# Kernel tuning notes

Hardware: AMD Instinct MI355X
Metric: run time of the kernel (lower is better)

The kernel has to match this reference:

```python
import jax, jax.numpy as jnp
import numpy as np

N = 100000      # nodes
E = 1600000     # edges
R = 8           # relations
D_IN = 64
D_H = 64
D_OUT = 64
G = 64          # graphs in batch


def setup_inputs() -> dict:
    key = jax.random.key(0)
    ks = jax.random.split(key, 10)
    x = jax.random.normal(ks[0], (N, D_IN), dtype=jnp.float32)
    edge_index = jax.random.randint(ks[1], (2, E), 0, N, dtype=jnp.int32)
    edge_type = jax.random.randint(ks[2], (E,), 0, R, dtype=jnp.int32)
    batch = jnp.sort(jax.random.randint(ks[3], (N,), 0, G, dtype=jnp.int32))
    s1 = 1.0 / np.sqrt(D_IN)
    s2 = 1.0 / np.sqrt(D_H)
    W1 = jax.random.normal(ks[4], (R, D_IN, D_H), dtype=jnp.float32) * s1
    root1 = jax.random.normal(ks[5], (D_IN, D_H), dtype=jnp.float32) * s1
    b1 = jnp.zeros((D_H,), dtype=jnp.float32)
    W2 = jax.random.normal(ks[6], (R, D_H, D_OUT), dtype=jnp.float32) * s2
    root2 = jax.random.normal(ks[7], (D_H, D_OUT), dtype=jnp.float32) * s2
    b2 = jnp.zeros((D_OUT,), dtype=jnp.float32)
    return {"x": x, "edge_index": edge_index, "edge_type": edge_type, "batch": batch,
            "W1": W1, "root1": root1, "b1": b1, "W2": W2, "root2": root2, "b2": b2}


def _rgcn_conv(x, src, dst, etype, W, root, b):
    # PyG RGCNConv (num_bases=None, aggr='mean'):
    #   out_i = sum_r mean_{j in N_r(i)} x_j @ W_r + x_i @ root + b
    # Aggregate-then-transform: per-(dst, relation) mean of source features,
    # then one einsum over relation weights.
    num_nodes, d = x.shape
    num_rel = W.shape[0]
    seg = dst * num_rel + etype                          # composite (node, rel) id
    sums = jax.ops.segment_sum(x[src], seg, num_segments=num_nodes * num_rel)
    cnt = jax.ops.segment_sum(jnp.ones_like(seg, dtype=x.dtype), seg,
                              num_segments=num_nodes * num_rel)
    mean = sums / jnp.maximum(cnt, 1.0)[:, None]         # [N*R, d]
    mean = mean.reshape(num_nodes, num_rel, d)           # [N, R, d]
    return jnp.einsum('nrd,rdh->nh', mean, W) + x @ root + b


def reference(x, edge_index, edge_type, batch, W1, root1, b1, W2, root2, b2):
    src, dst = edge_index[0], edge_index[1]
    h = jax.nn.relu(_rgcn_conv(x, src, dst, edge_type, W1, root1, b1))
    h = _rgcn_conv(h, src, dst, edge_type, W2, root2, b2)
    # global_mean_pool over graph ids
    gsum = jax.ops.segment_sum(h, batch, num_segments=G)
    gcnt = jax.ops.segment_sum(jnp.ones((h.shape[0],), h.dtype), batch, num_segments=G)
    return gsum / jnp.maximum(gcnt, 1.0)[:, None]
```

## Files before the change

kernel.cpp:

```cpp
#include <hip/hip_runtime.h>
#include <stdint.h>

typedef __attribute__((ext_vector_type(8))) short short8;
typedef __attribute__((ext_vector_type(4))) float floatx4;

__device__ inline float bf2f(unsigned short u) {
  union { unsigned int i; float f; } v; v.i = ((unsigned int)u) << 16; return v.f;
}
__device__ inline unsigned short f2bf(float f) {
  union { float f; unsigned int i; } v; v.f = f;
  unsigned int r = v.i + 0x7FFFu + ((v.i >> 16) & 1u);
  return (unsigned short)(r >> 16);
}

__global__ void zero_i32(int* __restrict__ p, int n) {
  int i = blockIdx.x * blockDim.x + threadIdx.x;
  if (i < n) p[i] = 0;
}

__global__ void count_rank(const int* __restrict__ dst, const int* __restrict__ et,
                           int* __restrict__ cnt, unsigned short* __restrict__ rank,
                           int E) {
  int e = blockIdx.x * blockDim.x + threadIdx.x;
  if (e < E) {
    int idx = dst[e] * 8 + et[e];
    rank[e] = (unsigned short)atomicAdd(&cnt[idx], 1);
  }
}

__global__ void invert_cnt(const int* __restrict__ cnt, float* __restrict__ inv, int n) {
  int i = blockIdx.x * blockDim.x + threadIdx.x;
  if (i < n) inv[i] = 1.0f / fmaxf((float)cnt[i], 1.0f);
}

#define SCAN_T 256
#define SCAN_E 4

__global__ void scan1(const int* __restrict__ cnt, int* __restrict__ bsum, int n) {
  __shared__ int lds[SCAN_T];
  int base = blockIdx.x * (SCAN_T * SCAN_E);
  int tid = threadIdx.x;
  int s = 0;
#pragma unroll
  for (int j = 0; j < SCAN_E; ++j) {
    int i = base + tid * SCAN_E + j;
    if (i < n) s += cnt[i];
  }
  lds[tid] = s; __syncthreads();
  for (int off = SCAN_T / 2; off > 0; off >>= 1) {
    if (tid < off) lds[tid] += lds[tid + off];
    __syncthreads();
  }
  if (tid == 0) bsum[blockIdx.x] = lds[0];
}

__global__ void scan2(int* __restrict__ bsum, int* __restrict__ eptr, int nb, int n) {
  __shared__ int lds[SCAN_T];
  int tid = threadIdx.x;
  int loc[4]; int s = 0;
#pragma unroll
  for (int j = 0; j < 4; ++j) {
    int i = tid * 4 + j;
    loc[j] = (i < nb) ? bsum[i] : 0; s += loc[j];
  }
  lds[tid] = s; __syncthreads();
  for (int off = 1; off < SCAN_T; off <<= 1) {
    int v = (tid >= off) ? lds[tid - off] : 0;
    __syncthreads();
    lds[tid] += v;
    __syncthreads();
  }
  int run = (tid > 0 ? lds[tid - 1] : 0);
#pragma unroll
  for (int j = 0; j < 4; ++j) {
    int i = tid * 4 + j;
    if (i < nb) { int v = loc[j]; bsum[i] = run; run += v; }
  }
  if (tid == 0) eptr[n] = lds[SCAN_T - 1];
}

__global__ void scan3(const int* __restrict__ cnt, const int* __restrict__ bsum,
                      int* __restrict__ eptr, int n) {
  __shared__ int lds[SCAN_T];
  int base = blockIdx.x * (SCAN_T * SCAN_E);
  int tid = threadIdx.x;
  int loc[SCAN_E]; int s = 0;
#pragma unroll
  for (int j = 0; j < SCAN_E; ++j) {
    int i = base + tid * SCAN_E + j;
    loc[j] = (i < n) ? cnt[i] : 0; s += loc[j];
  }
  lds[tid] = s; __syncthreads();
  for (int off = 1; off < SCAN_T; off <<= 1) {
    int v = (tid >= off) ? lds[tid - off] : 0;
    __syncthreads();
    lds[tid] += v;
    __syncthreads();
  }
  int run = (tid > 0 ? lds[tid - 1] : 0) + bsum[blockIdx.x];
#pragma unroll
  for (int j = 0; j < SCAN_E; ++j) {
    int i = base + tid * SCAN_E + j;
    if (i < n) { eptr[i] = run; run += loc[j]; }
  }
}

__global__ void scatter_edges(const int* __restrict__ src, const int* __restrict__ dst,
                              const int* __restrict__ et, const int* __restrict__ eptr8,
                              const unsigned short* __restrict__ rank,
                              unsigned* __restrict__ entry, int E) {
  int e = blockIdx.x * blockDim.x + threadIdx.x;
  if (e < E) {
    int d = dst[e], r = et[e];
    int p = eptr8[d * 8 + r] + (int)rank[e];
    entry[p] = ((unsigned)src[e] << 3) | (unsigned)r;
  }
}

__global__ void conv_weights(const float* __restrict__ W, const float* __restrict__ root,
                             unsigned short* __restrict__ Wb, int R) {
  int i = blockIdx.x * blockDim.x + threadIdx.x;
  int total = (R + 1) * 4096;
  if (i >= total) return;
  int m = i >> 12, rem = i & 4095, k = rem >> 6, c = rem & 63;
  float w = (m < R) ? W[(size_t)m * 4096 + k * 64 + c] : root[(size_t)k * 64 + c];
  int kc = k >> 5, q = (k >> 3) & 3, j = k & 7, nt = c >> 4, lcv = c & 15;
  Wb[(size_t)m * 4096 + (size_t)(((kc * 4 + q) * 4 + nt) * 16 + lcv) * 8 + j] = f2bf(w);
}

__global__ void __launch_bounds__(256)
transform_fused(const float* __restrict__ X, const unsigned short* __restrict__ Wb,
                const float* __restrict__ bias, unsigned short* __restrict__ Y,
                float* __restrict__ acc, int N, int relu_in)
{
  const int gy   = blockIdx.y;
  const int base = gy ? 4 : 0;
  const int ng   = gy ? 5 : 4;
  __shared__ __align__(16) unsigned short wlds[5 * 4096];

  const unsigned short* wsrc = Wb + (size_t)base * 4096;
  const int nel = ng * 4096;
  for (int i = threadIdx.x * 8; i < nel; i += 256 * 8)
    *(uint4*)&wlds[i] = *(const uint4*)&wsrc[i];
  __syncthreads();

  const int lane = threadIdx.x & 63;
  const int wave = threadIdx.x >> 6;
  const int lc   = lane & 15;
  const int quad = lane >> 4;
  const int tiles  = (N + 15) >> 4;
  const int stride = gridDim.x * 4;

  for (int t = blockIdx.x * 4 + wave; t < tiles; t += stride) {
    const int nb  = t << 4;
    const int row = min(nb + lc, N - 1);
    const float* xr = X + (size_t)row * 64;
    short8 a0, a1;
#pragma unroll
    for (int j = 0; j < 8; ++j) {
      float v0 = xr[quad * 8 + j];
      float v1 = xr[32 + quad * 8 + j];
      if (relu_in) { v0 = fmaxf(v0, 0.f); v1 = fmaxf(v1, 0.f); }
      a0[j] = (short)f2bf(v0);
      a1[j] = (short)f2bf(v1);
    }
    for (int gi = 0; gi < ng; ++gi) {
      const int g = base + gi;
#pragma unroll
      for (int nt = 0; nt < 4; ++nt) {
        short8 b0 = *(const short8*)&wlds[gi * 4096 + (((0 * 4 + quad) * 4 + nt) * 16 + lc) * 8];
        short8 b1 = *(const short8*)&wlds[gi * 4096 + (((1 * 4 + quad) * 4 + nt) * 16 + lc) * 8];
        floatx4 d = {0.f, 0.f, 0.f, 0.f};
        d = __builtin_amdgcn_mfma_f32_16x16x32_bf16(a0, b0, d, 0, 0, 0);
        d = __builtin_amdgcn_mfma_f32_16x16x32_bf16(a1, b1, d, 0, 0, 0);
        const int c = nt * 16 + lc;
        if (g < 8) {
#pragma unroll
          for (int i = 0; i < 4; ++i) {
            int r_ = nb + quad * 4 + i;
            if (r_ < N) Y[(size_t)r_ * 512 + g * 64 + c] = f2bf(d[i]);
          }
        } else {
          float bv = bias[c];
#pragma unroll
          for (int i = 0; i < 4; ++i) {
            int r_ = nb + quad * 4 + i;
            if (r_ < N) acc[(size_t)r_ * 64 + c] = d[i] + bv;
          }
        }
      }
    }
  }
}

__global__ void __launch_bounds__(256)
edge_agg_csr(const unsigned short* __restrict__ Y, const int* __restrict__ eptr8,
             const unsigned* __restrict__ entry, const float* __restrict__ inv,
             float* __restrict__ acc, int N)
{
  const int wid  = (blockIdx.x * blockDim.x + threadIdx.x) >> 6;
  const int lane = threadIdx.x & 63;
  if (wid >= N) return;
  const int lo = eptr8[wid * 8], hi = eptr8[wid * 8 + 8];
  const float invv = inv[(size_t)wid * 8 + (lane & 7)];
  float sum = 0.f;
  for (int base = lo; base < hi; base += 64) {
    const int rem = hi - base;
    const int mm = rem < 64 ? rem : 64;
    const unsigned en = entry[base + (lane < mm ? lane : mm - 1)];
    int j = 0;
    for (; j + 8 <= mm; j += 8) {
      unsigned e0 = __shfl(en, j),     e1 = __shfl(en, j + 1);
      unsigned e2 = __shfl(en, j + 2), e3 = __shfl(en, j + 3);
      unsigned e4 = __shfl(en, j + 4), e5 = __shfl(en, j + 5);
      unsigned e6 = __shfl(en, j + 6), e7 = __shfl(en, j + 7);
      float v0 = bf2f(Y[(size_t)(e0 >> 3) * 512 + (e0 & 7) * 64 + lane]);
      float v1 = bf2f(Y[(size_t)(e1 >> 3) * 512 + (e1 & 7) * 64 + lane]);
      float v2 = bf2f(Y[(size_t)(e2 >> 3) * 512 + (e2 & 7) * 64 + lane]);
      float v3 = bf2f(Y[(size_t)(e3 >> 3) * 512 + (e3 & 7) * 64 + lane]);
      float v4 = bf2f(Y[(size_t)(e4 >> 3) * 512 + (e4 & 7) * 64 + lane]);
      float v5 = bf2f(Y[(size_t)(e5 >> 3) * 512 + (e5 & 7) * 64 + lane]);
      float v6 = bf2f(Y[(size_t)(e6 >> 3) * 512 + (e6 & 7) * 64 + lane]);
      float v7 = bf2f(Y[(size_t)(e7 >> 3) * 512 + (e7 & 7) * 64 + lane]);
      sum += v0 * __shfl(invv, (int)(e0 & 7)) + v1 * __shfl(invv, (int)(e1 & 7))
           + v2 * __shfl(invv, (int)(e2 & 7)) + v3 * __shfl(invv, (int)(e3 & 7))
           + v4 * __shfl(invv, (int)(e4 & 7)) + v5 * __shfl(invv, (int)(e5 & 7))
           + v6 * __shfl(invv, (int)(e6 & 7)) + v7 * __shfl(invv, (int)(e7 & 7));
    }
    for (; j < mm; ++j) {
      unsigned e0 = __shfl(en, j);
      float v = bf2f(Y[(size_t)(e0 >> 3) * 512 + (e0 & 7) * 64 + lane]);
      sum += v * __shfl(invv, (int)(e0 & 7));
    }
  }
  acc[(size_t)wid * 64 + lane] += sum;
}

__global__ void glo_bounds(const int* __restrict__ batch, int* __restrict__ glo,
                           int N, int G) {
  int g = blockIdx.x * blockDim.x + threadIdx.x;
  if (g > G) return;
  if (g == G) { glo[G] = N; return; }
  int lo = 0, hi = N;
  while (lo < hi) { int mid = (lo + hi) >> 1; if (batch[mid] < g) lo = mid + 1; else hi = mid; }
  glo[g] = lo;
}

#define PS 24
__global__ void __launch_bounds__(256)
pool1(const float* __restrict__ acc, const int* __restrict__ glo,
      float* __restrict__ partial, int G)
{
  const int g = blockIdx.x;
  const int s = blockIdx.y;
  const int lane = threadIdx.x & 63;
  const int w = threadIdx.x >> 6;
  const int lo = glo[g], hi = glo[g + 1];
  const int len = hi - lo;
  const int a = lo + (int)(((long long)len * s) / PS);
  const int b = lo + (int)(((long long)len * (s + 1)) / PS);
  float sum = 0.f;
  for (int n = a + w; n < b; n += 4) sum += acc[(size_t)n * 64 + lane];
  __shared__ float red[4][64];
  red[w][lane] = sum;
  __syncthreads();
  if (w == 0)
    partial[((size_t)g * PS + s) * 64 + lane] =
        red[0][lane] + red[1][lane] + red[2][lane] + red[3][lane];
}

__global__ void pool2(const float* __restrict__ partial, const int* __restrict__ glo,
                      float* __restrict__ out, int G)
{
  const int g = blockIdx.x;
  const int lane = threadIdx.x;
  float t = 0.f;
#pragma unroll
  for (int s = 0; s < PS; ++s) t += partial[((size_t)g * PS + s) * 64 + lane];
  const int len = glo[g + 1] - glo[g];
  out[(size_t)g * 64 + lane] = t / fmaxf((float)len, 1.0f);
}

extern "C" void kernel_launch(void* const* d_in, const int* in_sizes, int n_in,
                              void* d_out, int out_size, void* d_ws, size_t ws_size,
                              hipStream_t stream)
{
  const float* x     = (const float*)d_in[0];
  const int*   ei    = (const int*)d_in[1];
  const int*   etype = (const int*)d_in[2];
  const int*   batch = (const int*)d_in[3];
  const float* W1    = (const float*)d_in[4];
  const float* root1 = (const float*)d_in[5];
  const float* b1    = (const float*)d_in[6];
  const float* W2    = (const float*)d_in[7];
  const float* root2 = (const float*)d_in[8];
  const float* b2    = (const float*)d_in[9];

  const int N = in_sizes[0] / 64;
  const int E = in_sizes[1] / 2;
  const int R = in_sizes[4] / (64 * 64);
  const int G = out_size / 64;
  const int* srcp = ei;
  const int* dstp = ei + E;
  const int n2 = N * R;

  char* ws = (char*)d_ws;
  size_t off = 0;
  auto carve = [&](size_t bytes) -> void* {
    void* p = ws + off; off = (off + bytes + 255) & ~(size_t)255; return p;
  };
  float*          inv     = (float*)carve((size_t)n2 * 4);
  float*          accA    = (float*)carve((size_t)N * 64 * 4);
  float*          accB    = (float*)carve((size_t)N * 64 * 4);
  unsigned short* Y       = (unsigned short*)carve((size_t)N * R * 64 * 2);
  int*            eptr8   = (int*)carve((size_t)(n2 + 1) * 4);
  unsigned*       entry   = (unsigned*)carve((size_t)E * 4);
  int*            bsum    = (int*)carve(1024 * 4);
  int*            glo     = (int*)carve((size_t)(G + 1) * 4);
  float*          partial = (float*)carve((size_t)G * PS * 64 * 4);
  unsigned short* Wb      = (unsigned short*)carve((size_t)(R + 1) * 4096 * 2);
  unsigned short* rank = (unsigned short*)accA;
  int*            cnt  = (int*)accB;
  (void)ws_size; (void)n_in;

  const int nb2 = (n2 + SCAN_T * SCAN_E - 1) / (SCAN_T * SCAN_E);

  zero_i32<<<(n2 + 255) / 256, 256, 0, stream>>>(cnt, n2);
  count_rank<<<(E + 255) / 256, 256, 0, stream>>>(dstp, etype, cnt, rank, E);
  invert_cnt<<<(n2 + 255) / 256, 256, 0, stream>>>(cnt, inv, n2);
  scan1<<<nb2, SCAN_T, 0, stream>>>(cnt, bsum, n2);
  scan2<<<1, SCAN_T, 0, stream>>>(bsum, eptr8, nb2, n2);
  scan3<<<nb2, SCAN_T, 0, stream>>>(cnt, bsum, eptr8, n2);
  scatter_edges<<<(E + 255) / 256, 256, 0, stream>>>(srcp, dstp, etype, eptr8, rank, entry, E);

  const int tiles = (N + 15) >> 4;
  dim3 tgrid((tiles + 3) / 4, 2);
  const int aggBlocks = (N * 64 + 255) / 256;
  const int wblocks = ((R + 1) * 4096 + 255) / 256;

  conv_weights<<<wblocks, 256, 0, stream>>>(W1, root1, Wb, R);
  transform_fused<<<tgrid, 256, 0, stream>>>(x, Wb, b1, Y, accA, N, 0);
  edge_agg_csr<<<aggBlocks, 256, 0, stream>>>(Y, eptr8, entry, inv, accA, N);

  conv_weights<<<wblocks, 256, 0, stream>>>(W2, root2, Wb, R);
  transform_fused<<<tgrid, 256, 0, stream>>>(accA, Wb, b2, Y, accB, N, 1);
  edge_agg_csr<<<aggBlocks, 256, 0, stream>>>(Y, eptr8, entry, inv, accB, N);

  glo_bounds<<<1, 128, 0, stream>>>(batch, glo, N, G);
  dim3 pgrid(G, PS);
  pool1<<<pgrid, 256, 0, stream>>>(accB, glo, partial, G);
  pool2<<<G, 64, 0, stream>>>(partial, glo, (float*)d_out, G);
}
```

Baseline: 433.6 us.

## Fuse prep kernels, overlap layer-1 transform with edge counting, drop small launches

```diff
diff --git a/kernel.cpp b/kernel.cpp
--- a/kernel.cpp
+++ b/kernel.cpp
@@ -13,24 +13,109 @@
   return (unsigned short)(r >> 16);
 }
 
-__global__ void zero_i32(int* __restrict__ p, int n) {
+__global__ void conv_prep(const float* __restrict__ W1, const float* __restrict__ root1,
+                          const float* __restrict__ W2, const float* __restrict__ root2,
+                          unsigned short* __restrict__ Wb, int* __restrict__ cnt, int n2)
+{
   int i = blockIdx.x * blockDim.x + threadIdx.x;
-  if (i < n) p[i] = 0;
-}
-
-__global__ void count_rank(const int* __restrict__ dst, const int* __restrict__ et,
-                           int* __restrict__ cnt, unsigned short* __restrict__ rank,
-                           int E) {
-  int e = blockIdx.x * blockDim.x + threadIdx.x;
-  if (e < E) {
-    int idx = dst[e] * 8 + et[e];
-    rank[e] = (unsigned short)atomicAdd(&cnt[idx], 1);
-  }
-}
-
-__global__ void invert_cnt(const int* __restrict__ cnt, float* __restrict__ inv, int n) {
-  int i = blockIdx.x * blockDim.x + threadIdx.x;
-  if (i < n) inv[i] = 1.0f / fmaxf((float)cnt[i], 1.0f);
+  if (i < 2 * 9 * 4096) {
+    int layer = i / 36864;
+    int rem = i - layer * 36864;
+    int m = rem >> 12, rem2 = rem & 4095, k = rem2 >> 6, c = rem2 & 63;
+    const float* Wm = layer ? W2 : W1;
+    const float* rt = layer ? root2 : root1;
+    float w = (m < 8) ? Wm[(size_t)m * 4096 + k * 64 + c] : rt[(size_t)k * 64 + c];
+    int kc = k >> 5, q = (k >> 3) & 3, j = k & 7, nt = c >> 4, lcv = c & 15;
+    Wb[(size_t)(layer * 9 + m) * 4096 + (size_t)(((kc * 4 + q) * 4 + nt) * 16 + lcv) * 8 + j] = f2bf(w);
+  } else {
+    int z = i - 2 * 9 * 4096;
+    if (z < n2) cnt[z] = 0;
+  }
+}
+
+__device__ __forceinline__ void transform_tile(
+    int t, int N, int lane, const float* __restrict__ X, int relu,
+    const unsigned short* __restrict__ Wb, const float* __restrict__ bias,
+    unsigned short* __restrict__ Y, float* __restrict__ accR)
+{
+  const int lc = lane & 15, quad = lane >> 4;
+  const int nb = t << 4;
+  const int row = min(nb + lc, N - 1);
+  const float* xr = X + (size_t)row * 64;
+  short8 a0, a1;
+#pragma unroll
+  for (int j = 0; j < 8; ++j) {
+    float v0 = xr[quad * 8 + j];
+    float v1 = xr[32 + quad * 8 + j];
+    if (relu) { v0 = fmaxf(v0, 0.f); v1 = fmaxf(v1, 0.f); }
+    a0[j] = (short)f2bf(v0);
+    a1[j] = (short)f2bf(v1);
+  }
+#pragma unroll
+  for (int g = 0; g < 9; ++g) {
+#pragma unroll
+    for (int nt = 0; nt < 4; ++nt) {
+      const short8 b0 = *(const short8*)&Wb[(size_t)g * 4096 +
+          (size_t)(((0 * 4 + quad) * 4 + nt) * 16 + lc) * 8];
+      const short8 b1 = *(const short8*)&Wb[(size_t)g * 4096 +
+          (size_t)(((1 * 4 + quad) * 4 + nt) * 16 + lc) * 8];
+      floatx4 d = {0.f, 0.f, 0.f, 0.f};
+      d = __builtin_amdgcn_mfma_f32_16x16x32_bf16(a0, b0, d, 0, 0, 0);
+      d = __builtin_amdgcn_mfma_f32_16x16x32_bf16(a1, b1, d, 0, 0, 0);
+      const int c = nt * 16 + lc;
+      if (g < 8) {
+#pragma unroll
+        for (int i = 0; i < 4; ++i) {
+          int r_ = nb + quad * 4 + i;
+          if (r_ < N) Y[(size_t)r_ * 512 + g * 64 + c] = f2bf(d[i]);
+        }
+      } else {
+        const float bv = bias[c];
+#pragma unroll
+        for (int i = 0; i < 4; ++i) {
+          int r_ = nb + quad * 4 + i;
+          if (r_ < N) accR[(size_t)r_ * 64 + c] = d[i] + bv;
+        }
+      }
+    }
+  }
+}
+
+__global__ void __launch_bounds__(256)
+count_and_t1(const int* __restrict__ dst, const int* __restrict__ et,
+             int* __restrict__ cnt, unsigned short* __restrict__ rank, int E,
+             const float* __restrict__ x, const unsigned short* __restrict__ Wb1,
+             const float* __restrict__ b1, unsigned short* __restrict__ Y,
+             float* __restrict__ accA, int N, int TB)
+{
+  const unsigned bx = blockIdx.x;
+  const bool isT = (bx % 5u == 0u) && (bx / 5u < (unsigned)TB);
+  if (isT) {
+    const int lane = threadIdx.x & 63;
+    const int wave = threadIdx.x >> 6;
+    const int t = (int)(bx / 5u) * 4 + wave;
+    if (t < ((N + 15) >> 4))
+      transform_tile(t, N, lane, x, 0, Wb1, b1, Y, accA);
+  } else {
+    const unsigned nT = min((bx + 4u) / 5u, (unsigned)TB);
+    const int e = (int)(bx - nT) * 256 + (int)threadIdx.x;
+    if (e < E) {
+      int idx = dst[e] * 8 + et[e];
+      rank[e] = (unsigned short)atomicAdd(&cnt[idx], 1);
+    }
+  }
+}
+
+__global__ void __launch_bounds__(256)
+transform_l2(const float* __restrict__ accA, const unsigned short* __restrict__ Wb2,
+             const float* __restrict__ b2, unsigned short* __restrict__ Y,
+             float* __restrict__ accB, int N)
+{
+  const int lane = threadIdx.x & 63;
+  const int wave = threadIdx.x >> 6;
+  const int t = blockIdx.x * 4 + wave;
+  if (t < ((N + 15) >> 4))
+    transform_tile(t, N, lane, accA, 1, Wb2, b2, Y, accB);
 }
 
 #define SCAN_T 256
@@ -117,92 +202,17 @@
   }
 }
 
-__global__ void conv_weights(const float* __restrict__ W, const float* __restrict__ root,
-                             unsigned short* __restrict__ Wb, int R) {
-  int i = blockIdx.x * blockDim.x + threadIdx.x;
-  int total = (R + 1) * 4096;
-  if (i >= total) return;
-  int m = i >> 12, rem = i & 4095, k = rem >> 6, c = rem & 63;
-  float w = (m < R) ? W[(size_t)m * 4096 + k * 64 + c] : root[(size_t)k * 64 + c];
-  int kc = k >> 5, q = (k >> 3) & 3, j = k & 7, nt = c >> 4, lcv = c & 15;
-  Wb[(size_t)m * 4096 + (size_t)(((kc * 4 + q) * 4 + nt) * 16 + lcv) * 8 + j] = f2bf(w);
-}
-
-__global__ void __launch_bounds__(256)
-transform_fused(const float* __restrict__ X, const unsigned short* __restrict__ Wb,
-                const float* __restrict__ bias, unsigned short* __restrict__ Y,
-                float* __restrict__ acc, int N, int relu_in)
-{
-  const int gy   = blockIdx.y;
-  const int base = gy ? 4 : 0;
-  const int ng   = gy ? 5 : 4;
-  __shared__ __align__(16) unsigned short wlds[5 * 4096];
-
-  const unsigned short* wsrc = Wb + (size_t)base * 4096;
-  const int nel = ng * 4096;
-  for (int i = threadIdx.x * 8; i < nel; i += 256 * 8)
-    *(uint4*)&wlds[i] = *(const uint4*)&wsrc[i];
-  __syncthreads();
-
-  const int lane = threadIdx.x & 63;
-  const int wave = threadIdx.x >> 6;
-  const int lc   = lane & 15;
-  const int quad = lane >> 4;
-  const int tiles  = (N + 15) >> 4;
-  const int stride = gridDim.x * 4;
-
-  for (int t = blockIdx.x * 4 + wave; t < tiles; t += stride) {
-    const int nb  = t << 4;
-    const int row = min(nb + lc, N - 1);
-    const float* xr = X + (size_t)row * 64;
-    short8 a0, a1;
-#pragma unroll
-    for (int j = 0; j < 8; ++j) {
-      float v0 = xr[quad * 8 + j];
-      float v1 = xr[32 + quad * 8 + j];
-      if (relu_in) { v0 = fmaxf(v0, 0.f); v1 = fmaxf(v1, 0.f); }
-      a0[j] = (short)f2bf(v0);
-      a1[j] = (short)f2bf(v1);
-    }
-    for (int gi = 0; gi < ng; ++gi) {
-      const int g = base + gi;
-#pragma unroll
-      for (int nt = 0; nt < 4; ++nt) {
-        short8 b0 = *(const short8*)&wlds[gi * 4096 + (((0 * 4 + quad) * 4 + nt) * 16 + lc) * 8];
-        short8 b1 = *(const short8*)&wlds[gi * 4096 + (((1 * 4 + quad) * 4 + nt) * 16 + lc) * 8];
-        floatx4 d = {0.f, 0.f, 0.f, 0.f};
-        d = __builtin_amdgcn_mfma_f32_16x16x32_bf16(a0, b0, d, 0, 0, 0);
-        d = __builtin_amdgcn_mfma_f32_16x16x32_bf16(a1, b1, d, 0, 0, 0);
-        const int c = nt * 16 + lc;
-        if (g < 8) {
-#pragma unroll
-          for (int i = 0; i < 4; ++i) {
-            int r_ = nb + quad * 4 + i;
-            if (r_ < N) Y[(size_t)r_ * 512 + g * 64 + c] = f2bf(d[i]);
-          }
-        } else {
-          float bv = bias[c];
-#pragma unroll
-          for (int i = 0; i < 4; ++i) {
-            int r_ = nb + quad * 4 + i;
-            if (r_ < N) acc[(size_t)r_ * 64 + c] = d[i] + bv;
-          }
-        }
-      }
-    }
-  }
-}
-
 __global__ void __launch_bounds__(256)
 edge_agg_csr(const unsigned short* __restrict__ Y, const int* __restrict__ eptr8,
-             const unsigned* __restrict__ entry, const float* __restrict__ inv,
-             float* __restrict__ acc, int N)
+             const unsigned* __restrict__ entry, float* __restrict__ acc, int N)
 {
   const int wid  = (blockIdx.x * blockDim.x + threadIdx.x) >> 6;
   const int lane = threadIdx.x & 63;
   if (wid >= N) return;
-  const int lo = eptr8[wid * 8], hi = eptr8[wid * 8 + 8];
-  const float invv = inv[(size_t)wid * 8 + (lane & 7)];
+  const int bv = eptr8[wid * 8 + (lane < 9 ? lane : 8)];
+  const int lo = __shfl(bv, 0), hi = __shfl(bv, 8);
+  const int wdt = __shfl(bv, (lane & 7) + 1) - __shfl(bv, lane & 7);
+  const float invv = 1.0f / (float)max(wdt, 1);
   float sum = 0.f;
   for (int base = lo; base < hi; base += 64) {
     const int rem = hi - base;
@@ -236,26 +246,23 @@
   acc[(size_t)wid * 64 + lane] += sum;
 }
 
-__global__ void glo_bounds(const int* __restrict__ batch, int* __restrict__ glo,
-                           int N, int G) {
-  int g = blockIdx.x * blockDim.x + threadIdx.x;
-  if (g > G) return;
-  if (g == G) { glo[G] = N; return; }
-  int lo = 0, hi = N;
-  while (lo < hi) { int mid = (lo + hi) >> 1; if (batch[mid] < g) lo = mid + 1; else hi = mid; }
-  glo[g] = lo;
+__device__ inline int lbound(const int* __restrict__ batch, int Nn, int g) {
+  int lo = 0, hi = Nn;
+  while (lo < hi) { int m = (lo + hi) >> 1; if (batch[m] < g) lo = m + 1; else hi = m; }
+  return lo;
 }
 
 #define PS 24
 __global__ void __launch_bounds__(256)
-pool1(const float* __restrict__ acc, const int* __restrict__ glo,
-      float* __restrict__ partial, int G)
+pool1(const float* __restrict__ acc, const int* __restrict__ batch,
+      float* __restrict__ partial, int N, int G)
 {
   const int g = blockIdx.x;
   const int s = blockIdx.y;
   const int lane = threadIdx.x & 63;
   const int w = threadIdx.x >> 6;
-  const int lo = glo[g], hi = glo[g + 1];
+  const int lo = lbound(batch, N, g);
+  const int hi = lbound(batch, N, g + 1);
   const int len = hi - lo;
   const int a = lo + (int)(((long long)len * s) / PS);
   const int b = lo + (int)(((long long)len * (s + 1)) / PS);
@@ -269,15 +276,15 @@
         red[0][lane] + red[1][lane] + red[2][lane] + red[3][lane];
 }
 
-__global__ void pool2(const float* __restrict__ partial, const int* __restrict__ glo,
-                      float* __restrict__ out, int G)
+__global__ void pool2(const float* __restrict__ partial, const int* __restrict__ batch,
+                      float* __restrict__ out, int N, int G)
 {
   const int g = blockIdx.x;
   const int lane = threadIdx.x;
   float t = 0.f;
 #pragma unroll
   for (int s = 0; s < PS; ++s) t += partial[((size_t)g * PS + s) * 64 + lane];
-  const int len = glo[g + 1] - glo[g];
+  const int len = lbound(batch, N, g + 1) - lbound(batch, N, g);
   out[(size_t)g * 64 + lane] = t / fmaxf((float)len, 1.0f);
 }
 
@@ -309,45 +316,42 @@
   auto carve = [&](size_t bytes) -> void* {
     void* p = ws + off; off = (off + bytes + 255) & ~(size_t)255; return p;
   };
-  float*          inv     = (float*)carve((size_t)n2 * 4);
   float*          accA    = (float*)carve((size_t)N * 64 * 4);
   float*          accB    = (float*)carve((size_t)N * 64 * 4);
   unsigned short* Y       = (unsigned short*)carve((size_t)N * R * 64 * 2);
   int*            eptr8   = (int*)carve((size_t)(n2 + 1) * 4);
   unsigned*       entry   = (unsigned*)carve((size_t)E * 4);
   int*            bsum    = (int*)carve(1024 * 4);
-  int*            glo     = (int*)carve((size_t)(G + 1) * 4);
   float*          partial = (float*)carve((size_t)G * PS * 64 * 4);
-  unsigned short* Wb      = (unsigned short*)carve((size_t)(R + 1) * 4096 * 2);
-  unsigned short* rank = (unsigned short*)accA;
+  unsigned short* Wb      = (unsigned short*)carve((size_t)2 * 9 * 4096 * 2);
   int*            cnt  = (int*)accB;
+  unsigned short* rank = (unsigned short*)((char*)accB + ((size_t)4 << 20));
   (void)ws_size; (void)n_in;
 
   const int nb2 = (n2 + SCAN_T * SCAN_E - 1) / (SCAN_T * SCAN_E);
-
-  zero_i32<<<(n2 + 255) / 256, 256, 0, stream>>>(cnt, n2);
-  count_rank<<<(E + 255) / 256, 256, 0, stream>>>(dstp, etype, cnt, rank, E);
-  invert_cnt<<<(n2 + 255) / 256, 256, 0, stream>>>(cnt, inv, n2);
+  const int tiles = (N + 15) >> 4;
+  const int TB = (tiles + 3) / 4;
+  const int CB = (E + 255) / 256;
+  const int prep_total = 2 * 9 * 4096 + n2;
+
+  conv_prep<<<(prep_total + 255) / 256, 256, 0, stream>>>(W1, root1, W2, root2, Wb, cnt, n2);
+
+  count_and_t1<<<CB + TB, 256, 0, stream>>>(dstp, etype, cnt, rank, E,
+                                            x, Wb, b1, Y, accA, N, TB);
+
   scan1<<<nb2, SCAN_T, 0, stream>>>(cnt, bsum, n2);
   scan2<<<1, SCAN_T, 0, stream>>>(bsum, eptr8, nb2, n2);
   scan3<<<nb2, SCAN_T, 0, stream>>>(cnt, bsum, eptr8, n2);
   scatter_edges<<<(E + 255) / 256, 256, 0, stream>>>(srcp, dstp, etype, eptr8, rank, entry, E);
 
-  const int tiles = (N + 15) >> 4;
-  dim3 tgrid((tiles + 3) / 4, 2);
   const int aggBlocks = (N * 64 + 255) / 256;
-  const int wblocks = ((R + 1) * 4096 + 255) / 256;
-
-  conv_weights<<<wblocks, 256, 0, stream>>>(W1, root1, Wb, R);
-  transform_fused<<<tgrid, 256, 0, stream>>>(x, Wb, b1, Y, accA, N, 0);
-  edge_agg_csr<<<aggBlocks, 256, 0, stream>>>(Y, eptr8, entry, inv, accA, N);
-
-  conv_weights<<<wblocks, 256, 0, stream>>>(W2, root2, Wb, R);
-  transform_fused<<<tgrid, 256, 0, stream>>>(accA, Wb, b2, Y, accB, N, 1);
-  edge_agg_csr<<<aggBlocks, 256, 0, stream>>>(Y, eptr8, entry, inv, accB, N);
-
-  glo_bounds<<<1, 128, 0, stream>>>(batch, glo, N, G);
+
+  edge_agg_csr<<<aggBlocks, 256, 0, stream>>>(Y, eptr8, entry, accA, N);
+
+  transform_l2<<<TB, 256, 0, stream>>>(accA, Wb + 9 * 4096, b2, Y, accB, N);
+  edge_agg_csr<<<aggBlocks, 256, 0, stream>>>(Y, eptr8, entry, accB, N);
+
   dim3 pgrid(G, PS);
-  pool1<<<pgrid, 256, 0, stream>>>(accB, glo, partial, G);
-  pool2<<<G, 64, 0, stream>>>(partial, glo, (float*)d_out, G);
-}
+  pool1<<<pgrid, 256, 0, stream>>>(accB, batch, partial, N, G);
+  pool2<<<G, 64, 0, stream>>>(partial, batch, (float*)d_out, N, G);
+}
```

Result: faster. 423.1 us (-2.4%).
